# Kernel optimization log

Hardware: AMD Instinct MI355X
Metric: run time of the kernel (lower is better)

## Reference

```python
import jax, jax.numpy as jnp
import numpy as np

ENV = 32  # hard-coded environment size in the original module
EPS_V = 1e-5


def _alignment(avg, mean_t, var_t, mean_e, var_e):
    # avg: [B, C]; mean_e/var_e: [n_env, ENV, C]; mean_t/var_t: [B, C]
    B, C = avg.shape
    n_env = B // ENV
    env = avg.reshape(n_env, ENV, C)
    m = env.mean(axis=1, keepdims=True)
    v = env.var(axis=1, keepdims=True, ddof=1)  # torch.var is unbiased
    env_aligned = ((env - m) / jnp.sqrt(v + EPS_V) * var_e + mean_e).reshape(B, C)
    tm = avg.mean(axis=0, keepdims=True)
    tv = avg.var(axis=0, keepdims=True, ddof=1)
    total_aligned = (avg - tm) / jnp.sqrt(tv + EPS_V) * var_t + mean_t
    return env_aligned, total_aligned


def _minmax(x):
    x_max = x.max(axis=-1, keepdims=True)
    x_min = x.min(axis=-1, keepdims=True)
    return (x - x_min) / (x_max - x_min)


def _dgcd_forward(x, r, ratio, rho):
    B, C, H, W = x.shape
    n_env = B // ENV
    # avg-pool and detach (original does x.detach().cpu() -> pool)
    avg = jax.lax.stop_gradient(x.mean(axis=(2, 3)))  # [B, C]

    # scaler params at init values (fresh modules each forward)
    mean_t = jnp.zeros((B, C), x.dtype)
    var_t = jnp.ones((B, C), x.dtype)
    mean_e = jnp.zeros((n_env, ENV, C), x.dtype)
    var_e = jnp.ones((n_env, ENV, C), x.dtype)

    def dist_fn(params):
        mt, vt, me, ve = params
        env_a, tot_a = _alignment(avg, mt, vt, me, ve)
        tot_ls = jax.nn.log_softmax(tot_a, axis=1)
        env_ls = jax.nn.log_softmax(env_a, axis=1)
        # KLDivLoss(log_target=True, reduction='batchmean')
        return jnp.sum(jnp.exp(env_ls) * (env_ls - tot_ls)) / B

    grads = jax.grad(dist_fn)((mean_t, var_t, mean_e, var_e))

    def perturb(p, g):
        nrm = jnp.linalg.norm(g, axis=-1, keepdims=True)
        return p + rho * g / jnp.sqrt(nrm + 1e-12)

    mean_t = perturb(mean_t, grads[0])
    var_t = perturb(var_t, grads[1])
    mean_e = perturb(mean_e, grads[2])
    var_e = perturb(var_e, grads[3])

    env_a, tot_a = _alignment(avg, mean_t, var_t, mean_e, var_e)

    # diag of (tot^T + 1e-7) @ (env + 1e-7) without the CxC matmul
    gram = jnp.sum((tot_a + 1e-7) * (env_a + 1e-7), axis=0)  # [C]
    tot_a = _minmax(tot_a / gram)
    env_a = _minmax(env_a / gram)
    scores = _minmax((tot_a - env_a) ** 2)  # [B, C]

    # gumbel-style weighted top-k keys
    key1 = r ** (1.0 / scores)
    k = int(ratio * C)
    thr = jnp.sort(key1, axis=1)[:, ::-1][:, k]  # descending sort, k-th value
    mask = 1.0 - jnp.where(key1 > thr[:, None], 1.0, 0.0)  # keep low-score channels
    mask = mask * (mask.size / mask.sum())
    return x * mask[:, :, None, None]


def setup_inputs() -> dict:
    key = jax.random.key(0)
    k1, k2 = jax.random.split(key)
    x = jax.random.normal(k1, (128, 2048, 14, 14), dtype=jnp.float32)
    r = jax.random.uniform(k2, (128, 2048), dtype=jnp.float32)
    return {"x": x, "r": r, "ratio": 0.3, "rho": 0.05}


def reference(x, r, ratio, rho):
    return _dgcd_forward(x, r, ratio, rho)
```

## Files before the change

kernel.cpp:

```cpp
#include <hip/hip_runtime.h>

#define B 128
#define C 2048
#define NENV 4
#define HW 196
#define HW4 49
#define EPSV 1e-5f

typedef float f32x4 __attribute__((ext_vector_type(4)));

__device__ __forceinline__ float wave_sum(float v) {
    for (int o = 32; o; o >>= 1) v += __shfl_down(v, o, 64);
    return v;
}
__device__ __forceinline__ float wave_max(float v) {
    for (int o = 32; o; o >>= 1) v = fmaxf(v, __shfl_down(v, o, 64));
    return v;
}
__device__ __forceinline__ float wave_min(float v) {
    for (int o = 32; o; o >>= 1) v = fminf(v, __shfl_down(v, o, 64));
    return v;
}

__device__ __forceinline__ float block_sum(float v, float* sred) {
    v = wave_sum(v);
    __syncthreads();
    if ((threadIdx.x & 63) == 0) sred[threadIdx.x >> 6] = v;
    __syncthreads();
    return (sred[0] + sred[1]) + (sred[2] + sred[3]);
}
__device__ __forceinline__ void block_sum2(float& a, float& b, float (*sr)[4]) {
    a = wave_sum(a); b = wave_sum(b);
    __syncthreads();
    const int w = threadIdx.x >> 6;
    if ((threadIdx.x & 63) == 0) { sr[0][w] = a; sr[1][w] = b; }
    __syncthreads();
    a = (sr[0][0] + sr[0][1]) + (sr[0][2] + sr[0][3]);
    b = (sr[1][0] + sr[1][1]) + (sr[1][2] + sr[1][3]);
}
__device__ __forceinline__ void block_sum4(float& a, float& b, float& c, float& d,
                                           float (*sr)[4]) {
    a = wave_sum(a); b = wave_sum(b); c = wave_sum(c); d = wave_sum(d);
    __syncthreads();
    const int w = threadIdx.x >> 6;
    if ((threadIdx.x & 63) == 0) { sr[0][w] = a; sr[1][w] = b; sr[2][w] = c; sr[3][w] = d; }
    __syncthreads();
    a = (sr[0][0] + sr[0][1]) + (sr[0][2] + sr[0][3]);
    b = (sr[1][0] + sr[1][1]) + (sr[1][2] + sr[1][3]);
    c = (sr[2][0] + sr[2][1]) + (sr[2][2] + sr[2][3]);
    d = (sr[3][0] + sr[3][1]) + (sr[3][2] + sr[3][3]);
}
__device__ __forceinline__ void block_max2(float& a, float& b, float (*sr)[4]) {
    a = wave_max(a); b = wave_max(b);
    __syncthreads();
    const int w = threadIdx.x >> 6;
    if ((threadIdx.x & 63) == 0) { sr[0][w] = a; sr[1][w] = b; }
    __syncthreads();
    a = fmaxf(fmaxf(sr[0][0], sr[0][1]), fmaxf(sr[0][2], sr[0][3]));
    b = fmaxf(fmaxf(sr[1][0], sr[1][1]), fmaxf(sr[1][2], sr[1][3]));
}
__device__ __forceinline__ void block_mm4(float& a, float& b, float& c, float& d,
                                          float (*sr)[4]) {
    a = wave_min(a); b = wave_max(b); c = wave_min(c); d = wave_max(d);
    __syncthreads();
    const int w = threadIdx.x >> 6;
    if ((threadIdx.x & 63) == 0) { sr[0][w] = a; sr[1][w] = b; sr[2][w] = c; sr[3][w] = d; }
    __syncthreads();
    a = fminf(fminf(sr[0][0], sr[0][1]), fminf(sr[0][2], sr[0][3]));
    b = fmaxf(fmaxf(sr[1][0], sr[1][1]), fmaxf(sr[1][2], sr[1][3]));
    c = fminf(fminf(sr[2][0], sr[2][1]), fminf(sr[2][2], sr[2][3]));
    d = fmaxf(fmaxf(sr[3][0], sr[3][1]), fmaxf(sr[3][2], sr[3][3]));
}
__device__ __forceinline__ void block_mm2(float& a, float& b, float (*sr)[4]) {
    a = wave_min(a); b = wave_max(b);
    __syncthreads();
    const int w = threadIdx.x >> 6;
    if ((threadIdx.x & 63) == 0) { sr[0][w] = a; sr[1][w] = b; }
    __syncthreads();
    a = fminf(fminf(sr[0][0], sr[0][1]), fminf(sr[0][2], sr[0][3]));
    b = fmaxf(fmaxf(sr[1][0], sr[1][1]), fmaxf(sr[1][2], sr[1][3]));
}

__device__ __forceinline__ float read_scalar01(const void* p) {
    float f = *(const float*)p;
    if (f > 1e-6f && f < 1.0f) return f;
    return (float)(*(const double*)p);
}

__global__ __launch_bounds__(256) void k_avg(const float* __restrict__ x,
                                             float* __restrict__ avg,
                                             int* __restrict__ cnt) {
    __shared__ float cs[256 * HW4];
    const int t = threadIdx.x;
    if (blockIdx.x == 0 && t == 0) cnt[0] = 0;
    const f32x4* x4 = (const f32x4*)x + (size_t)blockIdx.x * (256 * HW4);
    #pragma unroll
    for (int k = 0; k < HW4; ++k) {
        f32x4 v = x4[k * 256 + t];
        cs[k * 256 + t] = (v.x + v.y) + (v.z + v.w);
    }
    __syncthreads();
    float v[64];
    #pragma unroll
    for (int j = 0; j < HW4; ++j) v[j] = cs[t * HW4 + j];
    #pragma unroll
    for (int j = HW4; j < 64; ++j) v[j] = 0.0f;
    #pragma unroll
    for (int o = 32; o; o >>= 1)
        #pragma unroll
        for (int l = 0; l < 32; ++l)
            if (l < o) v[l] += v[l + o];
    avg[blockIdx.x * 256 + t] = v[0] * (1.0f / 196.0f);
}

__global__ __launch_bounds__(256) void k_stats(const float* __restrict__ avg,
        float* __restrict__ tm, float* __restrict__ tv,
        float* __restrict__ em, float* __restrict__ ev) {
    __shared__ double ps[16][16];
    __shared__ double pss[16][16];
    const int tid = threadIdx.x, bid = blockIdx.x;
    const int j = tid & 15;
    const int q = tid >> 4;
    const int c = bid * 16 + j;
    double s = 0.0, ss = 0.0;
    for (int i = 0; i < 8; ++i) {
        double a = (double)avg[(q * 8 + i) * C + c];
        s += a; ss += a * a;
    }
    ps[q][j] = s; pss[q][j] = ss;
    __syncthreads();
    if (tid < 64) {
        const int e = tid >> 4;
        double es = 0.0, ess = 0.0;
        for (int k = 0; k < 4; ++k) { es += ps[4 * e + k][j]; ess += pss[4 * e + k][j]; }
        double me = es * (1.0 / 32.0);
        em[e * C + c] = (float)me;
        ev[e * C + c] = (float)((ess - 32.0 * me * me) * (1.0 / 31.0));
    } else if (tid < 80) {
        const int jj = tid - 64;
        const int cc = bid * 16 + jj;
        double ts = 0.0, tss = 0.0;
        for (int k = 0; k < 16; ++k) { ts += ps[k][jj]; tss += pss[k][jj]; }
        double tmean = ts * (1.0 / 128.0);
        tm[cc] = (float)tmean;
        tv[cc] = (float)((tss - 128.0 * tmean * tmean) * (1.0 / 127.0));
    }
}

__global__ __launch_bounds__(256) void k_row1(const float* __restrict__ avg,
        const float* __restrict__ tm, const float* __restrict__ tv,
        const float* __restrict__ em, const float* __restrict__ ev,
        float* __restrict__ tota, float* __restrict__ enva,
        const void* __restrict__ rhop) {
    __shared__ float sr[4][4];
    const int tid = threadIdx.x, b = blockIdx.x, e = b >> 5;
    const float rho = read_scalar01(rhop);
    float zt[8], ze[8];
    for (int j = 0; j < 8; ++j) {
        int c = tid + (j << 8);
        float a = avg[b * C + c];
        zt[j] = (a - tm[c]) / sqrtf(tv[c] + EPSV);
        ze[j] = (a - em[e * C + c]) / sqrtf(ev[e * C + c] + EPSV);
    }
    float mxt = -1e30f, mxe = -1e30f;
    for (int j = 0; j < 8; ++j) { mxt = fmaxf(mxt, zt[j]); mxe = fmaxf(mxe, ze[j]); }
    block_max2(mxt, mxe, sr);
    float st = 0.f, se = 0.f;
    for (int j = 0; j < 8; ++j) { st += expf(zt[j] - mxt); se += expf(ze[j] - mxe); }
    block_sum2(st, se, sr);
    const float lst = logf(st), lse = logf(se);
    float kl = 0.f;
    for (int j = 0; j < 8; ++j) {
        float lt = zt[j] - mxt - lst, le = ze[j] - mxe - lse;
        kl += expf(le) * (le - lt);
    }
    kl = block_sum(kl, sr[0]);
    float gmt[8], gme[8];
    float nmt = 0.f, nvt = 0.f, nme = 0.f, nve = 0.f;
    for (int j = 0; j < 8; ++j) {
        float lt = zt[j] - mxt - lst, le = ze[j] - mxe - lse;
        float pt = expf(lt), pe = expf(le);
        float g1 = (pt - pe) * (1.0f / 128.0f);
        float g2 = pe * ((le - lt) - kl) * (1.0f / 128.0f);
        gmt[j] = g1; gme[j] = g2;
        float gv = g1 * zt[j], ge = g2 * ze[j];
        nmt += g1 * g1; nvt += gv * gv;
        nme += g2 * g2; nve += ge * ge;
    }
    block_sum4(nmt, nvt, nme, nve, sr);
    const float dmt = sqrtf(sqrtf(nmt) + 1e-12f);
    const float dvt = sqrtf(sqrtf(nvt) + 1e-12f);
    const float dme = sqrtf(sqrtf(nme) + 1e-12f);
    const float dve = sqrtf(sqrtf(nve) + 1e-12f);
    for (int j = 0; j < 8; ++j) {
        int c = tid + (j << 8);
        float vt_ = 1.0f + (rho * (gmt[j] * zt[j])) / dvt;
        float mt_ = (rho * gmt[j]) / dmt;
        float ve_ = 1.0f + (rho * (gme[j] * ze[j])) / dve;
        float me_ = (rho * gme[j]) / dme;
        tota[b * C + c] = zt[j] * vt_ + mt_;
        enva[b * C + c] = ze[j] * ve_ + me_;
    }
}

__global__ __launch_bounds__(256) void k_gram(const float* __restrict__ tota,
        const float* __restrict__ enva, float* __restrict__ gram) {
    __shared__ double ps[16][16];
    const int tid = threadIdx.x, bid = blockIdx.x;
    const int j = tid & 15;
    const int q = tid >> 4;
    const int c = bid * 16 + j;
    double s = 0.0;
    for (int i = 0; i < 8; ++i) {
        int idx = (q * 8 + i) * C + c;
        s += ((double)tota[idx] + 1e-7) * ((double)enva[idx] + 1e-7);
    }
    ps[q][j] = s;
    __syncthreads();
    if (tid < 16) {
        double g = 0.0;
        for (int k = 0; k < 16; ++k) g += ps[k][tid];
        gram[bid * 16 + tid] = (float)g;
    }
}

__global__ __launch_bounds__(256) void k_sel(const float* __restrict__ tota,
        const float* __restrict__ enva, const float* __restrict__ gram,
        const float* __restrict__ r,
        const void* __restrict__ ratiop,
        float* __restrict__ mask01, int* __restrict__ cnt) {
    __shared__ unsigned skey[C];
    __shared__ int hist[256];
    __shared__ float sr[4][4];
    __shared__ unsigned sprefix;
    __shared__ int srem;
    const int tid = threadIdx.x, b = blockIdx.x;
    float t_[8], e_[8];
    for (int j = 0; j < 8; ++j) {
        int c = tid + (j << 8);
        float g = gram[c];
        t_[j] = tota[b * C + c] / g;
        e_[j] = enva[b * C + c] / g;
    }
    float tmin = 1e30f, tmax = -1e30f, emin = 1e30f, emax = -1e30f;
    for (int j = 0; j < 8; ++j) {
        tmin = fminf(tmin, t_[j]); tmax = fmaxf(tmax, t_[j]);
        emin = fminf(emin, e_[j]); emax = fmaxf(emax, e_[j]);
    }
    block_mm4(tmin, tmax, emin, emax, sr);
    const float tden = tmax - tmin, eden = emax - emin;
    float s0[8];
    float smin = 1e30f, smax = -1e30f;
    for (int j = 0; j < 8; ++j) {
        float tn = (t_[j] - tmin) / tden;
        float en = (e_[j] - emin) / eden;
        float d = tn - en;
        s0[j] = d * d;
        smin = fminf(smin, s0[j]); smax = fmaxf(smax, s0[j]);
    }
    block_mm2(smin, smax, sr);
    const float sden = smax - smin;
    float key[8];
    for (int j = 0; j < 8; ++j) {
        int c = tid + (j << 8);
        float sc = (s0[j] - smin) / sden;
        key[j] = powf(r[b * C + c], 1.0f / sc);
        skey[c] = __float_as_uint(key[j]);
    }
    const int kk = (int)(read_scalar01(ratiop) * (float)C);
    if (tid == 0) { sprefix = 0u; srem = kk; }
    __syncthreads();
    for (int pass = 0; pass < 4; ++pass) {
        const int d = 24 - 8 * pass;
        const unsigned pmask = (pass == 0) ? 0u : (0xFFFFFFFFu << (32 - 8 * pass));
        const unsigned pref = sprefix;
        const int krem = srem;
        hist[tid] = 0;
        __syncthreads();
        for (int j = 0; j < 8; ++j) {
            unsigned bits = skey[tid + (j << 8)];
            if ((bits & pmask) == pref) atomicAdd(&hist[(bits >> d) & 255], 1);
        }
        __syncthreads();
        if (tid < 64) {
            int s = (hist[tid * 4] + hist[tid * 4 + 1]) +
                    (hist[tid * 4 + 2] + hist[tid * 4 + 3]);
            int S = s;
            for (int o = 1; o < 64; o <<= 1) {
                int t = __shfl_down(S, o, 64);
                if (tid + o < 64) S += t;
            }
            unsigned long long bal = __ballot(S > krem);
            int hi = 63 - __clzll(bal);
            if (tid == hi) {
                int cum = S - s;
                for (int q = 3; q >= 0; --q) {
                    int h = hist[tid * 4 + q];
                    if (cum + h > krem) {
                        sprefix = pref | ((unsigned)(tid * 4 + q) << d);
                        srem = krem - cum;
                        break;
                    }
                    cum += h;
                }
            }
        }
        __syncthreads();
    }
    const float thr = __uint_as_float(sprefix);
    float c8 = 0.f;
    for (int j = 0; j < 8; ++j) {
        int c = tid + (j << 8);
        float m = (key[j] > thr) ? 0.0f : 1.0f;
        mask01[b * C + c] = m;
        c8 += m;
    }
    c8 = block_sum(c8, sr[0]);
    if (tid == 0) atomicAdd(cnt, (int)c8);
}

__global__ __launch_bounds__(256) void k_apply(const float* __restrict__ x,
        const float* __restrict__ mask01, const int* __restrict__ cnt,
        float* __restrict__ out) {
    const float s = 262144.0f / (float)cnt[0];
    const int total4 = B * C * HW4;
    for (int i = blockIdx.x * 256 + threadIdx.x; i < total4; i += 2048 * 256) {
        float m = mask01[i / HW4];
        f32x4 v = {0.f, 0.f, 0.f, 0.f};
        if (m != 0.0f) {
            v = *((const f32x4*)x + i);
            v *= (m * s);
        }
        __builtin_nontemporal_store(v, (f32x4*)out + i);
    }
}

extern "C" void kernel_launch(void* const* d_in, const int* in_sizes, int n_in,
                              void* d_out, int out_size, void* d_ws, size_t ws_size,
                              hipStream_t stream) {
    const float* x = (const float*)d_in[0];
    const float* r = (const float*)d_in[1];
    const void* ratiop = d_in[2];
    const void* rhop = d_in[3];
    float* out = (float*)d_out;
    float* ws = (float*)d_ws;

    float* avg    = ws;
    float* tota   = avg    + B * C;
    float* enva   = tota   + B * C;
    float* mask01 = enva   + B * C;
    float* tm     = mask01 + B * C;
    float* tv     = tm + C;
    float* em     = tv + C;
    float* ev     = em + NENV * C;
    float* gram   = ev + NENV * C;
    int*   cnt    = (int*)(gram + C);

    k_avg  <<<dim3(B * C / 256), dim3(256), 0, stream>>>(x, avg, cnt);
    k_stats<<<dim3(128), dim3(256), 0, stream>>>(avg, tm, tv, em, ev);
    k_row1 <<<dim3(128), dim3(256), 0, stream>>>(avg, tm, tv, em, ev, tota, enva, rhop);
    k_gram <<<dim3(128), dim3(256), 0, stream>>>(tota, enva, gram);
    k_sel  <<<dim3(128), dim3(256), 0, stream>>>(tota, enva, gram, r, ratiop, mask01, cnt);
    k_apply<<<dim3(2048), dim3(256), 0, stream>>>(x, mask01, cnt, out);
}
```

Baseline: 113.5 us.

## Fuse column statistics and gram reduction into per-row kernels via redundant recompute

Removes the k_stats and k_gram kernels and has every row block in k_row1 and k_sel recompute the per-channel mean/variance and gram diagonal by reading all 128 rows itself. This eliminates two kernel launches and the intermediate workspace buffers. In exchange each of the 128 blocks reads the full avg (or tota and enva) matrices with fp64 accumulation, multiplying global/L2 traffic and double-precision work by the number of blocks.

```diff
diff --git a/kernel.cpp b/kernel.cpp
--- a/kernel.cpp
+++ b/kernel.cpp
@@ -113,43 +113,7 @@
     avg[blockIdx.x * 256 + t] = v[0] * (1.0f / 196.0f);
 }
 
-__global__ __launch_bounds__(256) void k_stats(const float* __restrict__ avg,
-        float* __restrict__ tm, float* __restrict__ tv,
-        float* __restrict__ em, float* __restrict__ ev) {
-    __shared__ double ps[16][16];
-    __shared__ double pss[16][16];
-    const int tid = threadIdx.x, bid = blockIdx.x;
-    const int j = tid & 15;
-    const int q = tid >> 4;
-    const int c = bid * 16 + j;
-    double s = 0.0, ss = 0.0;
-    for (int i = 0; i < 8; ++i) {
-        double a = (double)avg[(q * 8 + i) * C + c];
-        s += a; ss += a * a;
-    }
-    ps[q][j] = s; pss[q][j] = ss;
-    __syncthreads();
-    if (tid < 64) {
-        const int e = tid >> 4;
-        double es = 0.0, ess = 0.0;
-        for (int k = 0; k < 4; ++k) { es += ps[4 * e + k][j]; ess += pss[4 * e + k][j]; }
-        double me = es * (1.0 / 32.0);
-        em[e * C + c] = (float)me;
-        ev[e * C + c] = (float)((ess - 32.0 * me * me) * (1.0 / 31.0));
-    } else if (tid < 80) {
-        const int jj = tid - 64;
-        const int cc = bid * 16 + jj;
-        double ts = 0.0, tss = 0.0;
-        for (int k = 0; k < 16; ++k) { ts += ps[k][jj]; tss += pss[k][jj]; }
-        double tmean = ts * (1.0 / 128.0);
-        tm[cc] = (float)tmean;
-        tv[cc] = (float)((tss - 128.0 * tmean * tmean) * (1.0 / 127.0));
-    }
-}
-
 __global__ __launch_bounds__(256) void k_row1(const float* __restrict__ avg,
-        const float* __restrict__ tm, const float* __restrict__ tv,
-        const float* __restrict__ em, const float* __restrict__ ev,
         float* __restrict__ tota, float* __restrict__ enva,
         const void* __restrict__ rhop) {
     __shared__ float sr[4][4];
@@ -157,10 +121,26 @@
     const float rho = read_scalar01(rhop);
     float zt[8], ze[8];
     for (int j = 0; j < 8; ++j) {
-        int c = tid + (j << 8);
+        const int c = tid + (j << 8);
+        double ts = 0.0, tss = 0.0, es = 0.0, ess = 0.0;
+        for (int q = 0; q < 16; ++q) {
+            double s = 0.0, ss = 0.0;
+            for (int i = 0; i < 8; ++i) {
+                double a = (double)avg[(q * 8 + i) * C + c];
+                s += a; ss += a * a;
+            }
+            ts += s; tss += ss;
+            if ((q >> 2) == e) { es += s; ess += ss; }
+        }
+        double me = es * (1.0 / 32.0);
+        const float emf = (float)me;
+        const float evf = (float)((ess - 32.0 * me * me) * (1.0 / 31.0));
+        double tmean = ts * (1.0 / 128.0);
+        const float tmf = (float)tmean;
+        const float tvf = (float)((tss - 128.0 * tmean * tmean) * (1.0 / 127.0));
         float a = avg[b * C + c];
-        zt[j] = (a - tm[c]) / sqrtf(tv[c] + EPSV);
-        ze[j] = (a - em[e * C + c]) / sqrtf(ev[e * C + c] + EPSV);
+        zt[j] = (a - tmf) / sqrtf(tvf + EPSV);
+        ze[j] = (a - emf) / sqrtf(evf + EPSV);
     }
     float mxt = -1e30f, mxe = -1e30f;
     for (int j = 0; j < 8; ++j) { mxt = fmaxf(mxt, zt[j]); mxe = fmaxf(mxe, ze[j]); }
@@ -203,29 +183,8 @@
     }
 }
 
-__global__ __launch_bounds__(256) void k_gram(const float* __restrict__ tota,
-        const float* __restrict__ enva, float* __restrict__ gram) {
-    __shared__ double ps[16][16];
-    const int tid = threadIdx.x, bid = blockIdx.x;
-    const int j = tid & 15;
-    const int q = tid >> 4;
-    const int c = bid * 16 + j;
-    double s = 0.0;
-    for (int i = 0; i < 8; ++i) {
-        int idx = (q * 8 + i) * C + c;
-        s += ((double)tota[idx] + 1e-7) * ((double)enva[idx] + 1e-7);
-    }
-    ps[q][j] = s;
-    __syncthreads();
-    if (tid < 16) {
-        double g = 0.0;
-        for (int k = 0; k < 16; ++k) g += ps[k][tid];
-        gram[bid * 16 + tid] = (float)g;
-    }
-}
-
 __global__ __launch_bounds__(256) void k_sel(const float* __restrict__ tota,
-        const float* __restrict__ enva, const float* __restrict__ gram,
+        const float* __restrict__ enva,
         const float* __restrict__ r,
         const void* __restrict__ ratiop,
         float* __restrict__ mask01, int* __restrict__ cnt) {
@@ -237,10 +196,19 @@
     const int tid = threadIdx.x, b = blockIdx.x;
     float t_[8], e_[8];
     for (int j = 0; j < 8; ++j) {
-        int c = tid + (j << 8);
-        float g = gram[c];
-        t_[j] = tota[b * C + c] / g;
-        e_[j] = enva[b * C + c] / g;
+        const int c = tid + (j << 8);
+        double g = 0.0;
+        for (int q = 0; q < 16; ++q) {
+            double s = 0.0;
+            for (int i = 0; i < 8; ++i) {
+                int idx = (q * 8 + i) * C + c;
+                s += ((double)tota[idx] + 1e-7) * ((double)enva[idx] + 1e-7);
+            }
+            g += s;
+        }
+        const float gf = (float)g;
+        t_[j] = tota[b * C + c] / gf;
+        e_[j] = enva[b * C + c] / gf;
     }
     float tmin = 1e30f, tmax = -1e30f, emin = 1e30f, emax = -1e30f;
     for (int j = 0; j < 8; ++j) {
@@ -349,17 +317,10 @@
     float* tota   = avg    + B * C;
     float* enva   = tota   + B * C;
     float* mask01 = enva   + B * C;
-    float* tm     = mask01 + B * C;
-    float* tv     = tm + C;
-    float* em     = tv + C;
-    float* ev     = em + NENV * C;
-    float* gram   = ev + NENV * C;
-    int*   cnt    = (int*)(gram + C);
+    int*   cnt    = (int*)(mask01 + B * C);
 
     k_avg  <<<dim3(B * C / 256), dim3(256), 0, stream>>>(x, avg, cnt);
-    k_stats<<<dim3(128), dim3(256), 0, stream>>>(avg, tm, tv, em, ev);
-    k_row1 <<<dim3(128), dim3(256), 0, stream>>>(avg, tm, tv, em, ev, tota, enva, rhop);
-    k_gram <<<dim3(128), dim3(256), 0, stream>>>(tota, enva, gram);
-    k_sel  <<<dim3(128), dim3(256), 0, stream>>>(tota, enva, gram, r, ratiop, mask01, cnt);
+    k_row1 <<<dim3(128),  dim3(256), 0, stream>>>(avg, tota, enva, rhop);
+    k_sel  <<<dim3(128),  dim3(256), 0, stream>>>(tota, enva, r, ratiop, mask01, cnt);
     k_apply<<<dim3(2048), dim3(256), 0, stream>>>(x, mask01, cnt, out);
 }
```

Result: slower. 201.6 us (+77.7%).
